# Kernel optimization log

Measured on AMD Instinct MI355X. Metric: run time of the kernel, lower is better.

Reference implementation:

```python
import jax, jax.numpy as jnp
import numpy as np
from jax import lax

B, SEQ, PRED, CIN = 32, 336, 336, 7
ALL = SEQ + PRED
DM, DFF, NFFT, WIN, HOP = 64, 64, 64, 64, 8
NF = ALL // HOP + 1  # 85 STFT frames (center=True)
EL, CL, MARK = 2, 3, 4


def _conv2d(x, w, b, dil, pad):
    y = lax.conv_general_dilated(x, w, (1, 1), [(pad, pad), (pad, pad)],
                                 rhs_dilation=(dil, dil),
                                 dimension_numbers=('NCHW', 'OIHW', 'NCHW'))
    return y + b[None, :, None, None]


def _cconv(xr, xi, wr, wi, br, bi, dil, pad):
    # complex conv: (conv_r + i*conv_i)(xr + i*xi)
    rr = _conv2d(xr, wr, br, dil, pad)
    ii = _conv2d(xi, wi, bi, dil, pad)
    ri = _conv2d(xi, wr, br, dil, pad)
    ir = _conv2d(xr, wi, bi, dil, pad)
    return rr - ii, ri + ir


def _block(x, p):
    # x: [B, ALL, DM]; STFT per channel series (vectorized over B*DM, no python batch loop)
    xp = jnp.pad(x.transpose(0, 2, 1), ((0, 0), (0, 0), (NFFT // 2, NFFT // 2)), mode='reflect')
    idx = jnp.arange(NF)[:, None] * HOP + jnp.arange(NFFT)[None, :]
    win = 0.5 - 0.5 * jnp.cos(2.0 * jnp.pi * jnp.arange(WIN, dtype=jnp.float32) / WIN)  # periodic hann
    frames = xp[:, :, idx] * win  # [B, DM, NF, NFFT]
    S = jnp.fft.fft(frames, axis=-1) / jnp.sqrt(jnp.float32(NFFT))  # normalized=True (ortho)
    Sr = S.real.transpose(0, 1, 3, 2).astype(jnp.float32)  # [B, DM, NFFT, NF]
    Si = S.imag.transpose(0, 1, 3, 2).astype(jnp.float32)
    # complex 'qk' attention: compl_mul1d('ijxk,ijyk->ijxy', S, S)
    qk_r = jnp.einsum('bnxk,bnyk->bnxy', Sr, Sr) - jnp.einsum('bnxk,bnyk->bnxy', Si, Si)
    qk_i = jnp.einsum('bnxk,bnyk->bnxy', Sr, Si) + jnp.einsum('bnxk,bnyk->bnxy', Si, Sr)
    g_r = jax.nn.sigmoid(qk_r)
    g_i = jax.nn.sigmoid(qk_i)
    ar = jnp.einsum('bnxy,bnyz->bnxz', g_r, Sr) - jnp.einsum('bnxy,bnyz->bnxz', g_i, Si)
    ai = jnp.einsum('bnxy,bnyz->bnxz', g_r, Si) + jnp.einsum('bnxy,bnyz->bnxz', g_i, Sr)
    outs_r, outs_i = [], []
    yr, yi = _cconv(ar, ai, p['c0_wr'], p['c0_wi'], p['c0_br'], p['c0_bi'], 1, 0)
    outs_r.append(jax.nn.relu(yr)); outs_i.append(jax.nn.relu(yi))
    for k in range(1, CL):
        hr, hi = _cconv(ar, ai, p['cA_wr'][k - 1], p['cA_wi'][k - 1], p['cA_br'][k - 1], p['cA_bi'][k - 1], k, k)
        yr, yi = _cconv(hr, hi, p['cB_wr'][k - 1], p['cB_wi'][k - 1], p['cB_br'][k - 1], p['cB_bi'][k - 1], k, k)
        outs_r.append(jax.nn.relu(yr)); outs_i.append(jax.nn.relu(yi))
    mr = jnp.mean(jnp.stack(outs_r, -1), -1)
    mi = jnp.mean(jnp.stack(outs_i, -1), -1)
    y = mr * p['l0_w'][0, 0] + mi * p['l0_w'][0, 1] + p['l0_b'][0]  # Linear(2 -> 1) over (real, imag)
    y = y.mean(axis=2)  # mean over freq axis -> [B, DM, NF]
    y = jnp.einsum('bnf,af->bna', y, p['l2_w']) + p['l2_b']  # l2: NF -> ALL
    return y.transpose(0, 2, 1)  # [B, ALL, DM]


def _ln(x, g, b):
    m = x.mean(-1, keepdims=True)
    v = ((x - m) ** 2).mean(-1, keepdims=True)
    return (x - m) / jnp.sqrt(v + 1e-5) * g + b


def _forward(x_enc, x_mark_enc, tok_w, temp_w, pl_w, pl_b, ln_g, ln_b,
             c0_wr, c0_wi, c0_br, c0_bi, cA_wr, cA_wi, cA_br, cA_bi,
             cB_wr, cB_wi, cB_br, cB_bi, l0_w, l0_b, l2_w, l2_b,
             cv_w, cv_b, l1_w, l1_b, proj_w, proj_b):
    means = x_enc.mean(1, keepdims=True)
    xe = x_enc - means
    stdev = jnp.sqrt(xe.var(axis=1, keepdims=True) + 1e-5)
    xe = xe / stdev
    # DataEmbedding: circular token conv + sinusoidal PE + timeF linear (dropout=0)
    xv = jnp.pad(xe.transpose(0, 2, 1), ((0, 0), (0, 0), (1, 1)), mode='wrap')
    val = lax.conv_general_dilated(xv, tok_w, (1,), [(0, 0)],
                                   dimension_numbers=('NCH', 'OIH', 'NCH')).transpose(0, 2, 1)
    pos = jnp.arange(SEQ, dtype=jnp.float32)[:, None]
    div = jnp.exp(jnp.arange(0, DM, 2, dtype=jnp.float32) * (-np.log(10000.0) / DM))
    pe = jnp.zeros((SEQ, DM), jnp.float32).at[:, 0::2].set(jnp.sin(pos * div)).at[:, 1::2].set(jnp.cos(pos * div))
    enc = val + x_mark_enc @ temp_w.T + pe
    enc = jnp.einsum('btd,at->bad', enc, pl_w) + pl_b[None, :, None]  # predict_linear over time axis
    for l in range(EL):
        p = dict(c0_wr=c0_wr[l], c0_wi=c0_wi[l], c0_br=c0_br[l], c0_bi=c0_bi[l],
                 cA_wr=cA_wr[l], cA_wi=cA_wi[l], cA_br=cA_br[l], cA_bi=cA_bi[l],
                 cB_wr=cB_wr[l], cB_wi=cB_wi[l], cB_br=cB_br[l], cB_bi=cB_bi[l],
                 l0_w=l0_w[l], l0_b=l0_b[l], l2_w=l2_w[l], l2_b=l2_b[l])
        enc = _ln(_block(enc, p), ln_g, ln_b)
    # conv1d(in=ALL channels, kernel 3, stride 2, pad 1) over the d_model axis, then l1
    h = lax.conv_general_dilated(enc, cv_w, (2,), [(1, 1)],
                                 dimension_numbers=('NCH', 'OIH', 'NCH')) + cv_b[None, :, None]
    seq_series = (h @ l1_w.T)[..., 0] + l1_b[0]  # [B, ALL]
    dec = enc @ proj_w.T + proj_b
    dec = dec * stdev + means
    return dec[:, -PRED:, :], seq_series


def setup_inputs():
    key = jax.random.key(0)
    ks = jax.random.split(key, 24)
    def r(i, shape, s=0.02):
        return jax.random.normal(ks[i], shape, dtype=jnp.float32) * s
    return {
        'x_enc': jax.random.normal(ks[0], (B, SEQ, CIN), dtype=jnp.float32),
        'x_mark_enc': jax.random.normal(ks[1], (B, SEQ, MARK), dtype=jnp.float32),
        'x_dec': jax.random.normal(ks[2], (B, 48 + PRED, CIN), dtype=jnp.float32),
        'x_mark_dec': jax.random.normal(ks[3], (B, 48 + PRED, MARK), dtype=jnp.float32),
        'tok_w': r(4, (DM, CIN, 3), 0.1),
        'temp_w': r(5, (DM, MARK), 0.1),
        'pl_w': r(6, (ALL, SEQ), 0.05),
        'pl_b': jnp.zeros((ALL,), jnp.float32),
        'ln_g': jnp.ones((DM,), jnp.float32),
        'ln_b': jnp.zeros((DM,), jnp.float32),
        'c0_wr': r(7, (EL, DM, DM, 1, 1), 0.05),
        'c0_wi': r(8, (EL, DM, DM, 1, 1), 0.05),
        'c0_br': jnp.zeros((EL, DM), jnp.float32),
        'c0_bi': jnp.zeros((EL, DM), jnp.float32),
        'cA_wr': r(9, (EL, CL - 1, DFF, DM, 3, 3), 0.02),
        'cA_wi': r(10, (EL, CL - 1, DFF, DM, 3, 3), 0.02),
        'cA_br': jnp.zeros((EL, CL - 1, DFF), jnp.float32),
        'cA_bi': jnp.zeros((EL, CL - 1, DFF), jnp.float32),
        'cB_wr': r(11, (EL, CL - 1, DM, DFF, 3, 3), 0.02),
        'cB_wi': r(12, (EL, CL - 1, DM, DFF, 3, 3), 0.02),
        'cB_br': jnp.zeros((EL, CL - 1, DM), jnp.float32),
        'cB_bi': jnp.zeros((EL, CL - 1, DM), jnp.float32),
        'l0_w': r(13, (EL, 1, 2), 0.5),
        'l0_b': jnp.zeros((EL, 1), jnp.float32),
        'l2_w': r(14, (EL, ALL, NF), 0.05),
        'l2_b': jnp.zeros((EL, ALL), jnp.float32),
        'cv_w': r(15, (ALL, ALL, 3), 0.02),
        'cv_b': jnp.zeros((ALL,), jnp.float32),
        'l1_w': r(16, (1, DM // 2), 0.1),
        'l1_b': jnp.zeros((1,), jnp.float32),
        'proj_w': r(17, (CIN, DM), 0.1),
        'proj_b': jnp.zeros((CIN,), jnp.float32),
    }


def reference(x_enc, x_mark_enc, x_dec, x_mark_dec, tok_w, temp_w, pl_w, pl_b, ln_g, ln_b,
              c0_wr, c0_wi, c0_br, c0_bi, cA_wr, cA_wi, cA_br, cA_bi,
              cB_wr, cB_wi, cB_br, cB_bi, l0_w, l0_b, l2_w, l2_b,
              cv_w, cv_b, l1_w, l1_b, proj_w, proj_b):
    del x_dec, x_mark_dec  # unused in the forecast path
    return _forward(x_enc, x_mark_enc, tok_w, temp_w, pl_w, pl_b, ln_g, ln_b,
                    c0_wr, c0_wi, c0_br, c0_bi, cA_wr, cA_wi, cA_br, cA_bi,
                    cB_wr, cB_wi, cB_br, cB_bi, l0_w, l0_b, l2_w, l2_b,
                    cv_w, cv_b, l1_w, l1_b, proj_w, proj_b)
```

## Files before the change

kernel.cpp:

```cpp
#include <hip/hip_runtime.h>

typedef __attribute__((ext_vector_type(8))) short short8v;
typedef __attribute__((ext_vector_type(4))) float f32x4;
typedef __attribute__((ext_vector_type(16))) float f32x16;

static constexpr int Bt = 32;
static constexpr int SEQ = 336, PRED = 336, CIN = 7, ALLT = 672;
static constexpr int DM = 64, NFFT = 64, HOP = 8, NF = 85;
static constexpr int MARK = 4;
static constexpr float INV3 = 1.0f / 3.0f;

__device__ inline short f2bf(float v) {
    unsigned u = __float_as_uint(v);
    u += 0x7fffu + ((u >> 16) & 1u);
    return (short)(u >> 16);
}
__device__ inline float bf2f(short h) {
    return __uint_as_float(((unsigned)(unsigned short)h) << 16);
}
__device__ inline int pack2(float r, float i) {
    return ((int)(unsigned short)f2bf(r)) | (((int)(unsigned short)f2bf(i)) << 16);
}
__device__ inline void async16(const int* g, short* l) {
    __builtin_amdgcn_global_load_lds(
        (const __attribute__((address_space(1))) unsigned int*)g,
        (__attribute__((address_space(3))) unsigned int*)l, 16, 0, 0);
}

__global__ __launch_bounds__(64) void k_stats(const float* __restrict__ x,
                                              float* __restrict__ mean,
                                              float* __restrict__ stdv) {
    int bc = blockIdx.x;
    int b = bc / CIN, c = bc % CIN;
    int lane = threadIdx.x;
    float s = 0.f, s2 = 0.f;
    for (int t = lane; t < SEQ; t += 64) {
        float v = x[(b * SEQ + t) * CIN + c];
        s += v; s2 += v * v;
    }
    for (int m = 32; m >= 1; m >>= 1) { s += __shfl_xor(s, m); s2 += __shfl_xor(s2, m); }
    if (lane == 0) {
// ... 55 lines not shown
        for (int r = 0; r < 4; ++r) acc[q][r] = 0.f;
    for (int tc = 0; tc < 6; ++tc) {
        if (tc) __syncthreads();
        for (int i = tid; i < 56 * 64; i += 256)
            Et[i] = enc0[((size_t)b * SEQ + tc * 56) * DM + i];
        for (int i = tid; i < 48 * 56; i += 256) {
            int r = i / 56, c = i - r * 56;
            Wt[c * 49 + r] = pl_w[(size_t)(abase + r) * SEQ + tc * 56 + c];
        }
        __syncthreads();
#pragma unroll 4
        for (int t = 0; t < 56; ++t) {
            float4 e = *(const float4*)&Et[t * 64 + d0];
            float w0 = Wt[t * 49 + a0];
            float w1 = Wt[t * 49 + a0 + 1];
            float w2 = Wt[t * 49 + a0 + 2];
            acc[0][0] += w0 * e.x; acc[0][1] += w0 * e.y;
            acc[0][2] += w0 * e.z; acc[0][3] += w0 * e.w;
            acc[1][0] += w1 * e.x; acc[1][1] += w1 * e.y;
            acc[1][2] += w1 * e.z; acc[1][3] += w1 * e.w;
            acc[2][0] += w2 * e.x; acc[2][1] += w2 * e.y;
            acc[2][2] += w2 * e.z; acc[2][3] += w2 * e.w;
        }
    }
#pragma unroll
    for (int q = 0; q < 3; ++q) {
        int a = abase + a0 + q;
        float bias = pl_b[a];
        float4 o = {acc[q][0] + bias, acc[q][1] + bias, acc[q][2] + bias, acc[q][3] + bias};
        *(float4*)&enc[((size_t)b * ALLT + a) * DM + d0] = o;
    }
}

__global__ __launch_bounds__(256) void k_stqka(const float* __restrict__ enc, int b0,
                                               int* __restrict__ Apk) {
    __shared__ __align__(16) short L[54272];
    constexpr int TCH = 0, TCL = 4608, TSH = 9216, TSL = 13824;
    constexpr int XWH = 18432, XWL = 25344;
    float* xp  = (float*)&L[32256];
    float* twc = (float*)&L[33728];
    float* tws = (float*)&L[33984];
    constexpr int SRH = 0, SIH = 6656, SRL = 13312, SIL = 19968;
    constexpr int STRH = 26624, STRL = 33536, STIH = 40448, STIL = 47360;
    constexpr int GRH = 0, GRL = 4608, GIH = 9216, GIL = 13824;

    int blk = blockIdx.x;
    int bn = (blk & 7) * (gridDim.x >> 3) + (blk >> 3);
    int bl = bn >> 6, n = bn & 63;
    int bg = b0 + bl;
    int tid = threadIdx.x;
    int lane = tid & 63, w = tid >> 6;
    int l31 = lane & 31, kg = lane >> 5;

    for (int i = tid; i < ALLT + NFFT; i += 256) {
        int j = i - 32;
        if (j < 0) j = -j;
        if (j > ALLT - 1) j = 2 * (ALLT - 1) - j;
        xp[i] = enc[((size_t)bg * ALLT + j) * DM + n];
    }
    if (tid < 64) {
        float ang = (6.283185307179586f / 64.f) * (float)tid;
        twc[tid] = cosf(ang);
        tws[tid] = sinf(ang);
    }
    __syncthreads();
    for (int i = tid; i < 64 * 64; i += 256) {
        int k = i >> 6, tt = i & 63;
        int m = (k * tt) & 63;
        float c = twc[m], s = tws[m];
        short ch = f2bf(c); short cl = f2bf(c - bf2f(ch));
        short sh = f2bf(s); short sl = f2bf(s - bf2f(sh));
        int o = k * 72 + tt;
        L[TCH + o] = ch; L[TCL + o] = cl; L[TSH + o] = sh; L[TSL + o] = sl;
    }
    for (int i = tid; i < 96 * 64; i += 256) {
        int f = i >> 6, tt = i & 63;
        float v = 0.f;
        if (f < 85) v = xp[f * HOP + tt] * (0.5f - 0.5f * twc[tt]) * 0.125f;
        short vh = f2bf(v); short vl = f2bf(v - bf2f(vh));
        int o = f * 72 + tt;
        L[XWH + o] = vh; L[XWL + o] = vl;
    }
    __syncthreads();

    int kt = w & 1;
    int ftA = (w < 2) ? 0 : 2;
    f32x16 srA, siA, srB, siB;
#pragma unroll
    for (int r = 0; r < 16; ++r) { srA[r] = 0.f; siA[r] = 0.f; srB[r] = 0.f; siB[r] = 0.f; }
#pragma unroll
    for (int tts = 0; tts < 4; ++tts) {
        int ko = (kt * 32 + l31) * 72 + tts * 16 + kg * 8;
        short8v ach = *(const short8v*)&L[TCH + ko];
        short8v acl = *(const short8v*)&L[TCL + ko];
        short8v ash = *(const short8v*)&L[TSH + ko];
        short8v asl = *(const short8v*)&L[TSL + ko];
        {
            int bo = (ftA * 32 + l31) * 72 + tts * 16 + kg * 8;
            short8v bh = *(const short8v*)&L[XWH + bo];
            short8v bl_ = *(const short8v*)&L[XWL + bo];
            srA = __builtin_amdgcn_mfma_f32_32x32x16_bf16(ach, bh, srA, 0, 0, 0);
            srA = __builtin_amdgcn_mfma_f32_32x32x16_bf16(acl, bh, srA, 0, 0, 0);
            srA = __builtin_amdgcn_mfma_f32_32x32x16_bf16(ach, bl_, srA, 0, 0, 0);
            siA = __builtin_amdgcn_mfma_f32_32x32x16_bf16(ash, bh, siA, 0, 0, 0);
            siA = __builtin_amdgcn_mfma_f32_32x32x16_bf16(asl, bh, siA, 0, 0, 0);
            siA = __builtin_amdgcn_mfma_f32_32x32x16_bf16(ash, bl_, siA, 0, 0, 0);
        }
        if (w < 2) {
            int bo = (32 + l31) * 72 + tts * 16 + kg * 8;
            short8v bh = *(const short8v*)&L[XWH + bo];
            short8v bl_ = *(const short8v*)&L[XWL + bo];
            srB = __builtin_amdgcn_mfma_f32_32x32x16_bf16(ach, bh, srB, 0, 0, 0);
            srB = __builtin_amdgcn_mfma_f32_32x32x16_bf16(acl, bh, srB, 0, 0, 0);
            srB = __builtin_amdgcn_mfma_f32_32x32x16_bf16(ach, bl_, srB, 0, 0, 0);
            siB = __builtin_amdgcn_mfma_f32_32x32x16_bf16(ash, bh, siB, 0, 0, 0);
            siB = __builtin_amdgcn_mfma_f32_32x32x16_bf16(asl, bh, siB, 0, 0, 0);
            siB = __builtin_amdgcn_mfma_f32_32x32x16_bf16(ash, bl_, siB, 0, 0, 0);
        }
    }
    __syncthreads();

    {
        int fA = ftA * 32 + l31;
#pragma unroll
        for (int rg = 0; rg < 4; ++rg) {
            int k0 = kt * 32 + 8 * rg + 4 * kg;
            short prh[4], prl[4], pih[4], pil[4];
#pragma unroll
            for (int q = 0; q < 4; ++q) {
                int r = rg * 4 + q;
                float sv = srA[r], iv = -siA[r];
                short rh = f2bf(sv); short rl = f2bf(sv - bf2f(rh));
                short ih = f2bf(iv); short il = f2bf(iv - bf2f(ih));
                prh[q] = rh; prl[q] = rl; pih[q] = ih; pil[q] = il;
                L[SRH + (k0 + q) * 104 + fA] = rh; L[SRL + (k0 + q) * 104 + fA] = rl;
                L[SIH + (k0 + q) * 104 + fA] = ih; L[SIL + (k0 + q) * 104 + fA] = il;
            }
            *(long long*)&L[STRH + fA * 72 + k0] = *(long long*)prh;
            *(long long*)&L[STRL + fA * 72 + k0] = *(long long*)prl;
            *(long long*)&L[STIH + fA * 72 + k0] = *(long long*)pih;
            *(long long*)&L[STIL + fA * 72 + k0] = *(long long*)pil;
        }
        if (w < 2) {
            int fB = 32 + l31;
#pragma unroll
            for (int rg = 0; rg < 4; ++rg) {
                int k0 = kt * 32 + 8 * rg + 4 * kg;
                short prh[4], prl[4], pih[4], pil[4];
#pragma unroll
                for (int q = 0; q < 4; ++q) {
                    int r = rg * 4 + q;
                    float sv = srB[r], iv = -siB[r];
                    short rh = f2bf(sv); short rl = f2bf(sv - bf2f(rh));
                    short ih = f2bf(iv); short il = f2bf(iv - bf2f(ih));
                    prh[q] = rh; prl[q] = rl; pih[q] = ih; pil[q] = il;
                    L[SRH + (k0 + q) * 104 + fB] = rh; L[SRL + (k0 + q) * 104 + fB] = rl;
                    L[SIH + (k0 + q) * 104 + fB] = ih; L[SIL + (k0 + q) * 104 + fB] = il;
                }
                *(long long*)&L[STRH + fB * 72 + k0] = *(long long*)prh;
                *(long long*)&L[STRL + fB * 72 + k0] = *(long long*)prl;
                *(long long*)&L[STIH + fB * 72 + k0] = *(long long*)pih;
                *(long long*)&L[STIL + fB * 72 + k0] = *(long long*)pil;
            }
        }
    }
    __syncthreads();

    int mh = w >> 1, nh = w & 1;
    f32x16 P, Q, R;
#pragma unroll
    for (int r = 0; r < 16; ++r) { P[r] = 0.f; Q[r] = 0.f; R[r] = 0.f; }
#pragma unroll
    for (int f0 = 0; f0 < 96; f0 += 16) {
        int ka = f0 + kg * 8;
        int ra = (mh * 32 + l31) * 104 + ka;
        int rb = (nh * 32 + l31) * 104 + ka;
        short8v a_rh = *(const short8v*)&L[SRH + ra];
        short8v a_rl = *(const short8v*)&L[SRL + ra];
        short8v a_ih = *(const short8v*)&L[SIH + ra];
        short8v a_il = *(const short8v*)&L[SIL + ra];
        short8v b_rh = *(const short8v*)&L[SRH + rb];
        short8v b_rl = *(const short8v*)&L[SRL + rb];
        short8v b_ih = *(const short8v*)&L[SIH + rb];
        short8v b_il = *(const short8v*)&L[SIL + rb];
        P = __builtin_amdgcn_mfma_f32_32x32x16_bf16(a_rh, b_rh, P, 0, 0, 0);
        P = __builtin_amdgcn_mfma_f32_32x32x16_bf16(a_rl, b_rh, P, 0, 0, 0);
        P = __builtin_amdgcn_mfma_f32_32x32x16_bf16(a_rh, b_rl, P, 0, 0, 0);
        Q = __builtin_amdgcn_mfma_f32_32x32x16_bf16(a_ih, b_ih, Q, 0, 0, 0);
        Q = __builtin_amdgcn_mfma_f32_32x32x16_bf16(a_il, b_ih, Q, 0, 0, 0);
        Q = __builtin_amdgcn_mfma_f32_32x32x16_bf16(a_ih, b_il, Q, 0, 0, 0);
        R = __builtin_amdgcn_mfma_f32_32x32x16_bf16(a_rh, b_ih, R, 0, 0, 0);
        R = __builtin_amdgcn_mfma_f32_32x32x16_bf16(a_rl, b_ih, R, 0, 0, 0);
        R = __builtin_amdgcn_mfma_f32_32x32x16_bf16(a_rh, b_il, R, 0, 0, 0);
        R = __builtin_amdgcn_mfma_f32_32x32x16_bf16(a_ih, b_rh, R, 0, 0, 0);
        R = __builtin_amdgcn_mfma_f32_32x32x16_bf16(a_il, b_rh, R, 0, 0, 0);
        R = __builtin_amdgcn_mfma_f32_32x32x16_bf16(a_ih, b_rl, R, 0, 0, 0);
    }
    __syncthreads();

    {
        int y = nh * 32 + l31;
#pragma unroll
        for (int r = 0; r < 16; ++r) {
            int x = mh * 32 + (r & 3) + 8 * (r >> 2) + 4 * kg;
            float gr = 1.f / (1.f + __expf(-(P[r] - Q[r])));
            float gi = 1.f / (1.f + __expf(-R[r]));
            short gh = f2bf(gr); short gl = f2bf(gr - bf2f(gh));
            short jh = f2bf(gi); short jl = f2bf(gi - bf2f(jh));
            L[GRH + x * 72 + y] = gh; L[GRL + x * 72 + y] = gl;
            L[GIH + x * 72 + y] = jh; L[GIL + x * 72 + y] = jl;
        }
    }
    __syncthreads();

    int mg = w >> 1;
    int mtA = (mg == 0) ? 0 : 2;
    f32x16 u1A, u2A, u3A, u1B, u2B, u3B;
#pragma unroll
    for (int r = 0; r < 16; ++r) {
        u1A[r] = 0.f; u2A[r] = 0.f; u3A[r] = 0.f;
        u1B[r] = 0.f; u2B[r] = 0.f; u3B[r] = 0.f;
    }
#pragma unroll
    for (int y0 = 0; y0 < 64; y0 += 16) {
        int kb = y0 + kg * 8;
        int gb = (nh * 32 + l31) * 72 + kb;
        short8v bgrh = *(const short8v*)&L[GRH + gb];
        short8v bgrl = *(const short8v*)&L[GRL + gb];
        short8v bgih = *(const short8v*)&L[GIH + gb];
        short8v bgil = *(const short8v*)&L[GIL + gb];
        {
            int sa = (mtA * 32 + l31) * 72 + kb;
            short8v arh = *(const short8v*)&L[STRH + sa];
            short8v arl = *(const short8v*)&L[STRL + sa];
            short8v aih = *(const short8v*)&L[STIH + sa];
            short8v ail = *(const short8v*)&L[STIL + sa];
            u1A = __builtin_amdgcn_mfma_f32_32x32x16_bf16(arh, bgrh, u1A, 0, 0, 0);
            u1A = __builtin_amdgcn_mfma_f32_32x32x16_bf16(arl, bgrh, u1A, 0, 0, 0);
            u1A = __builtin_amdgcn_mfma_f32_32x32x16_bf16(arh, bgrl, u1A, 0, 0, 0);
            u2A = __builtin_amdgcn_mfma_f32_32x32x16_bf16(aih, bgih, u2A, 0, 0, 0);
            u2A = __builtin_amdgcn_mfma_f32_32x32x16_bf16(ail, bgih, u2A, 0, 0, 0);
            u2A = __builtin_amdgcn_mfma_f32_32x32x16_bf16(aih, bgil, u2A, 0, 0, 0);
            u3A = __builtin_amdgcn_mfma_f32_32x32x16_bf16(aih, bgrh, u3A, 0, 0, 0);
            u3A = __builtin_amdgcn_mfma_f32_32x32x16_bf16(ail, bgrh, u3A, 0, 0, 0);
            u3A = __builtin_amdgcn_mfma_f32_32x32x16_bf16(aih, bgrl, u3A, 0, 0, 0);
            u3A = __builtin_amdgcn_mfma_f32_32x32x16_bf16(arh, bgih, u3A, 0, 0, 0);
            u3A = __builtin_amdgcn_mfma_f32_32x32x16_bf16(arl, bgih, u3A, 0, 0, 0);
            u3A = __builtin_amdgcn_mfma_f32_32x32x16_bf16(arh, bgil, u3A, 0, 0, 0);
        }
        if (mg == 0) {
            int sa = (1 * 32 + l31) * 72 + kb;
            short8v arh = *(const short8v*)&L[STRH + sa];
            short8v arl = *(const short8v*)&L[STRL + sa];
            short8v aih = *(const short8v*)&L[STIH + sa];
            short8v ail = *(const short8v*)&L[STIL + sa];
            u1B = __builtin_amdgcn_mfma_f32_32x32x16_bf16(arh, bgrh, u1B, 0, 0, 0);
            u1B = __builtin_amdgcn_mfma_f32_32x32x16_bf16(arl, bgrh, u1B, 0, 0, 0);
            u1B = __builtin_amdgcn_mfma_f32_32x32x16_bf16(arh, bgrl, u1B, 0, 0, 0);
            u2B = __builtin_amdgcn_mfma_f32_32x32x16_bf16(aih, bgih, u2B, 0, 0, 0);
            u2B = __builtin_amdgcn_mfma_f32_32x32x16_bf16(ail, bgih, u2B, 0, 0, 0);
            u2B = __builtin_amdgcn_mfma_f32_32x32x16_bf16(aih, bgil, u2B, 0, 0, 0);
            u3B = __builtin_amdgcn_mfma_f32_32x32x16_bf16(aih, bgrh, u3B, 0, 0, 0);
            u3B = __builtin_amdgcn_mfma_f32_32x32x16_bf16(ail, bgrh, u3B, 0, 0, 0);
            u3B = __builtin_amdgcn_mfma_f32_32x32x16_bf16(aih, bgrl, u3B, 0, 0, 0);
            u3B = __builtin_amdgcn_mfma_f32_32x32x16_bf16(arh, bgih, u3B, 0, 0, 0);
            u3B = __builtin_amdgcn_mfma_f32_32x32x16_bf16(arl, bgih, u3B, 0, 0, 0);
            u3B = __builtin_amdgcn_mfma_f32_32x32x16_bf16(arh, bgil, u3B, 0, 0, 0);
        }
    }
    {
        size_t pkbase = ((size_t)(bl * 16 + (n >> 2)) * 64) * 85 * 4 + (n & 3);
        int x2 = nh * 32 + l31;
#pragma unroll
        for (int r = 0; r < 16; ++r) {
            int z = mtA * 32 + (r & 3) + 8 * (r >> 2) + 4 * kg;
            if (z < 85)
                Apk[pkbase + ((size_t)x2 * 85 + z) * 4] = pack2(u1A[r] - u2A[r], u3A[r]);
        }
        if (mg == 0) {
#pragma unroll
            for (int r = 0; r < 16; ++r) {
                int z = 32 + (r & 3) + 8 * (r >> 2) + 4 * kg;
                Apk[pkbase + ((size_t)x2 * 85 + z) * 4] = pack2(u1B[r] - u2B[r], u3B[r]);
            }
        }
    }
}

__global__ __launch_bounds__(256) void k_wprep(const float* __restrict__ cA_wr,
                                               const float* __restrict__ cA_wi,
                                               const float* __restrict__ cB_wr,
                                               const float* __restrict__ cB_wi,
                                               const float* __restrict__ c0_wr,
                                               const float* __restrict__ c0_wi,
                                               short* __restrict__ wt) {
    int idx = blockIdx.x * 256 + threadIdx.x;
    if (idx >= 1245184) return;
    int c32 = idx & 31;
    int m = (idx >> 5) & 127;
    int ci_l = c32 >> 1;
    int part = c32 & 1;
    int co = m & 63;
    const float *wr, *wi;
    size_t woff;
    bool lo = false;
    int chunk;
    if (idx < 1179648) {
        chunk = (idx >> 12) & 3;
        int tap = (idx >> 14) % 9;
        int conv = idx / 147456;
        int l = conv >> 2, k1 = (conv >> 1) & 1, ab = conv & 1;
        int ci = chunk * 16 + ci_l;
        woff = (((size_t)(l * 2 + k1) * 64 + co) * 64 + ci) * 9 + tap;
        wr = ab ? cB_wr : cA_wr;
        wi = ab ? cB_wi : cA_wi;
    } else {
        int i2 = idx - 1179648;
        chunk = (i2 >> 12) & 3;
        lo = (i2 >> 14) & 1;
        int l = i2 >> 15;
        int ci = chunk * 16 + ci_l;
        woff = ((size_t)(l * 64 + co)) * 64 + ci;
        wr = c0_wr; wi = c0_wi;
    }
    float a = wr[woff], bb = wi[woff];
    float v = (m < 64) ? (part ? -bb : a) : (part ? a : bb);
    if (lo) v = v - bf2f(f2bf(v));
    wt[idx] = f2bf(v);
}

__global__ __launch_bounds__(256, 4) void k_conv3p(const int* __restrict__ in_pk,
                                                   const short* __restrict__ wt,
                                                   const float* __restrict__ b_r,
                                                   const float* __restrict__ b_i,
                                                   int K, int mode,
                                                   const float* __restrict__ l0w,
                                                   int* __restrict__ out_pk,
                                                   float* __restrict__ yfull) {
    __shared__ __align__(16) short inT[2][1020 * 8];
    int blk = blockIdx.x;
    int swz = (blk & 7) * (gridDim.x >> 3) + (blk >> 3);
    int b = swz >> 6, x0 = swz & 63;
    int tid = threadIdx.x;
    int lane = tid & 63, wid = tid >> 6;
    int wrow = wid & 1, wcol = wid >> 1;
    int l15 = lane & 15, g = lane >> 4;

#define STAGE(CC, BUFI)                                                       \
    do {                                                                      \
        _Pragma("unroll")                                                     \
        for (int it = 0; it < 4; ++it) {                                      \
            int idx = tid + it * 256;                                         \
            if (idx < 1020) {                                                 \
                int f = idx % 85;                                             \
                int rc = idx / 85;                                            \
                int xr = rc >> 2, cg = rc & 3;                                \
                int xg = x0 + (xr - 1) * K;                                   \
                if ((unsigned)xg < 64u) {                                     \
                    const int* src = in_pk +                                  \
                        (((size_t)((b * 16 + (CC) * 4 + cg) * 64 + xg)) * 85 + f) * 4; \
                    async16(src, &inT[BUFI][(wid * 64 + it * 256) * 8]);      \
                }                                                             \
            }                                                                 \
        }                                                                     \
    } while (0)

    { int* p = (int*)&inT[0][0];
      for (int i = tid; i < 2 * 1020 * 4; i += 256) p[i] = 0; }
    __syncthreads();

    f32x4 acc[4][3];
#pragma unroll
    for (int a = 0; a < 4; ++a)
#pragma unroll
        for (int j = 0; j < 3; ++j) acc[a][j] = f32x4{0.f, 0.f, 0.f, 0.f};

    STAGE(0, 0);
    __syncthreads();

    int cur = 0;
    for (int chunk = 0; chunk < 4; ++chunk) {
        if (chunk == 0) STAGE(1, 1);
        else if (chunk == 1) STAGE(2, 0);
        else if (chunk == 2) STAGE(3, 1);
        const short* bb = &inT[cur][0];
#pragma unroll
        for (int u = 0; u < 3; ++u) {
#pragma unroll
            for (int v = 0; v < 3; ++v) {
                int tap = u * 3 + v;
                short8v afr[4];
#pragma unroll
                for (int a = 0; a < 4; ++a) {
                    int tile = (a < 2) ? (wrow * 2 + a) : (wrow * 2 + a + 2);
                    const short* ap = wt + ((((size_t)tap * 4 + chunk) * 8 + tile) * 16 + l15) * 32 + g * 8;
                    afr[a] = *(const short8v*)ap;
                }
                short8v bfr[3];
#pragma unroll
                for (int j = 0; j < 3; ++j) {
                    int fs = (wcol * 3 + j) * 16 + l15 + (v - 1) * K;
                    bool inr = ((unsigned)fs < 85u);
                    int fsc = inr ? fs : 0;
                    short8v t8 = *(const short8v*)&bb[((u * 4 + g) * 85 + fsc) * 8];
                    bfr[j] = inr ? t8 : short8v{0, 0, 0, 0, 0, 0, 0, 0};
                }
#pragma unroll
                for (int a = 0; a < 4; ++a)
#pragma unroll
                    for (int j = 0; j < 3; ++j)
                        acc[a][j] = __builtin_amdgcn_mfma_f32_16x16x32_bf16(afr[a], bfr[j],
                                                                            acc[a][j], 0, 0, 0);
            }
        }
        __syncthreads();
        cur ^= 1;
    }
#undef STAGE

    float w0 = 0.f, w1 = 0.f;
    if (mode == 1) { w0 = l0w[0]; w1 = l0w[1]; }
#pragma unroll
    for (int a = 0; a < 2; ++a) {
#pragma unroll
        for (int j = 0; j < 3; ++j) {
            int f = (wcol * 3 + j) * 16 + l15;
            if (f < NF) {
                if (mode == 0) {
                    int4 o;
#pragma unroll
                    for (int reg = 0; reg < 4; ++reg) {
                        int co = (wrow * 2 + a) * 16 + g * 4 + reg;
                        float vrq = acc[a][j][reg]     + b_r[co] - b_i[co];
                        float viq = acc[a + 2][j][reg] + b_r[co] + b_i[co];
                        ((int*)&o)[reg] = pack2(vrq, viq);
                    }
                    int co4 = (wrow * 2 + a) * 4 + g;
                    ((int4*)out_pk)[((size_t)((b * 16 + co4) * 64 + x0)) * 85 + f] = o;
                } else {
#pragma unroll
                    for (int reg = 0; reg < 4; ++reg) {
                        int co = (wrow * 2 + a) * 16 + g * 4 + reg;
                        float vrq = acc[a][j][reg]     + b_r[co] - b_i[co];
                        float viq = acc[a + 2][j][reg] + b_r[co] + b_i[co];
                        size_t o = ((size_t)(b * 64 + co) * 64 + x0) * NF + f;
                        yfull[o] += (fmaxf(vrq, 0.f) * w0 + fmaxf(viq, 0.f) * w1) * INV3;
                    }
                }
            }
        }
    }
}

__global__ __launch_bounds__(256, 4) void k_c0m(const int* __restrict__ Apk,
                                                const short* __restrict__ wt,
                                                const float* __restrict__ b_r,
                                                const float* __restrict__ b_i,
                                                const float* __restrict__ l0w,
                                                float* __restrict__ yfull) {
    __shared__ __align__(16) short inT[100 * 40];
    int blk = blockIdx.x;
    int swz = (blk & 7) * (gridDim.x >> 3) + (blk >> 3);
    int b = swz >> 6, x0 = swz & 63;
    int tid = threadIdx.x;
    int lane = tid & 63, wid = tid >> 6;
    int wrow = wid & 1, wcol = wid >> 1;
    int l15 = lane & 15, g = lane >> 4;

    f32x4 acc[4][3];
#pragma unroll
    for (int a = 0; a < 4; ++a)
#pragma unroll
        for (int j = 0; j < 3; ++j) acc[a][j] = f32x4{0.f, 0.f, 0.f, 0.f};

    for (int chunk = 0; chunk < 4; ++chunk) {
        if (chunk > 0) __syncthreads();
        for (int idx = tid; idx < 340; idx += 256) {
            int f = idx % 85;
            int cg = idx / 85;
            size_t s4 = ((size_t)((b * 16 + chunk * 4 + cg) * 64 + x0)) * 85 + f;
            int4 dh = ((const int4*)Apk)[s4];
            *(int4*)&inT[(f + 2) * 40 + cg * 8] = dh;
        }
        __syncthreads();
#pragma unroll
        for (int wtap = 0; wtap < 2; ++wtap) {
            short8v afr[4];
#pragma unroll
            for (int a = 0; a < 4; ++a) {
                int tile = (a < 2) ? (wrow * 2 + a) : (wrow * 2 + a + 2);
                const short* ap = wt + ((((size_t)wtap * 4 + chunk) * 8 + tile) * 16 + l15) * 32 + g * 8;
                afr[a] = *(const short8v*)ap;
            }
            short8v bfr[3];
#pragma unroll
            for (int j = 0; j < 3; ++j) {
                int fs = (wcol * 3 + j) * 16 + l15 + 2;
                bfr[j] = *(const short8v*)&inT[fs * 40 + g * 8];
            }
#pragma unroll
            for (int a = 0; a < 4; ++a)
#pragma unroll
                for (int j = 0; j < 3; ++j)
                    acc[a][j] = __builtin_amdgcn_mfma_f32_16x16x32_bf16(afr[a], bfr[j],
                                                                        acc[a][j], 0, 0, 0);
        }
    }

    float w0 = l0w[0], w1 = l0w[1];
#pragma unroll
    for (int a = 0; a < 2; ++a) {
#pragma unroll
        for (int j = 0; j < 3; ++j) {
            int f = (wcol * 3 + j) * 16 + l15;
            if (f < NF) {
// ... 122 lines not shown
    const float* c0_br  = (const float*)d_in[12];
    const float* c0_bi  = (const float*)d_in[13];
    const float* cA_wr  = (const float*)d_in[14];
    const float* cA_wi  = (const float*)d_in[15];
    const float* cA_br  = (const float*)d_in[16];
    const float* cA_bi  = (const float*)d_in[17];
    const float* cB_wr  = (const float*)d_in[18];
    const float* cB_wi  = (const float*)d_in[19];
    const float* cB_br  = (const float*)d_in[20];
    const float* cB_bi  = (const float*)d_in[21];
    const float* l0_w   = (const float*)d_in[22];
    const float* l0_b   = (const float*)d_in[23];
    const float* l2_w   = (const float*)d_in[24];
    const float* l2_b   = (const float*)d_in[25];
    const float* cv_w   = (const float*)d_in[26];
    const float* cv_b   = (const float*)d_in[27];
    const float* l1_w   = (const float*)d_in[28];
    const float* l1_b   = (const float*)d_in[29];
    const float* proj_w = (const float*)d_in[30];
    const float* proj_b = (const float*)d_in[31];

    float* out0 = (float*)d_out;
    float* out1 = out0 + (size_t)Bt * PRED * CIN;

    float* ws = (float*)d_ws;
    size_t off = 0;
    float* enc  = ws + off; off += (size_t)Bt * ALLT * DM;
    float* enc0 = ws + off; off += (size_t)Bt * SEQ * DM;
    float* mean = ws + off; off += 256;
    float* stdv = ws + off; off += 256;
    short* wtbuf = (short*)(ws + off); off += 622592;

    const size_t perb = (size_t)DM * NFFT * NF;
    int Bc = 32;
    while (Bc > 1) {
        size_t need = (off + (size_t)Bc * DM * NF + 3 * (size_t)Bc * perb) * sizeof(float);
        if (need <= ws_size) break;
        Bc >>= 1;
    }
    float* y2 = ws + off; off += (size_t)Bc * DM * NF;
    float* yfull = ws + off; off += (size_t)Bc * perb;
    int*   Apk = (int*)(ws + off); off += (size_t)Bc * perb;
    int*   Hpk = (int*)(ws + off); off += (size_t)Bc * perb;
    float* Tb = enc0;

    k_stats<<<Bt * CIN, 64, 0, stream>>>(x_enc, mean, stdv);
    k_wprep<<<(1245184 + 255) / 256, 256, 0, stream>>>(cA_wr, cA_wi, cB_wr, cB_wi,
                                                       c0_wr, c0_wi, wtbuf);
    k_embed<<<(Bt * SEQ * DM + 255) / 256, 256, 0, stream>>>(x_enc, x_mark, tok_w, temp_w,
                                                             mean, stdv, enc0);
    k_plin2<<<Bt * 14, 256, 0, stream>>>(enc0, pl_w, pl_b, enc);

    for (int l = 0; l < 2; ++l) {
        for (int b0 = 0; b0 < Bt; b0 += Bc) {
            k_stqka<<<Bc * 64, 256, 0, stream>>>(enc, b0, Apk);
            k_c0m<<<Bc * 64, 256, 0, stream>>>(Apk, wtbuf + 1179648 + (size_t)l * 32768,
                                               c0_br + l * 64, c0_bi + l * 64,
                                               l0_w + l * 2, yfull);
            for (int k = 1; k <= 2; ++k) {
                int convA = l * 4 + (k - 1) * 2;
                size_t boff = ((size_t)l * 2 + (k - 1)) * 64;
                k_conv3p<<<Bc * 64, 256, 0, stream>>>(Apk, wtbuf + (size_t)convA * 147456,
                                                      cA_br + boff, cA_bi + boff, k, 0,
                                                      l0_w + l * 2, Hpk, yfull);
                k_conv3p<<<Bc * 64, 256, 0, stream>>>(Hpk, wtbuf + (size_t)(convA + 1) * 147456,
                                                      cB_br + boff, cB_bi + boff, k, 1,
                                                      l0_w + l * 2, Hpk, yfull);
            }
            k_reduce2<<<Bc * 64, 256, 0, stream>>>(yfull, l0_b + l, y2);
            k_l2ln<<<Bc * ALLT, 64, 0, stream>>>(y2, l2_w + (size_t)l * ALLT * NF,
                                                 l2_b + (size_t)l * ALLT, ln_g, ln_b, enc, b0);
        }
    }

    k_T<<<(Bt * ALLT * 3 + 255) / 256, 256, 0, stream>>>(enc, l1_w, Tb);
    k_seq<<<(Bt * ALLT + 255) / 256, 256, 0, stream>>>(Tb, cv_w, cv_b, l1_w, l1_b, out1);
    k_dec<<<(Bt * PRED * CIN + 255) / 256, 256, 0, stream>>>(enc, proj_w, proj_b, mean, stdv, out0);
}
```

Before: 1.369 ms.

## Pad frame dimension of packed activations and widen STFT-attention kernel to 512 threads

The packed complex activation buffers (Apk/Hpk) now use a padded frame stride of 100 with a 2-element zero halo, zeroed once by a memset. This removes bounds checks and conditional zeroing in the conv kernels' B-fragment loads and the reshuffling offset in k_c0m. Separately, k_stqka runs 8 waves so the STFT and the attention-output GEMM tiles each go to their own wave, instead of some waves doing double tiles. The trade-off is more memory traffic for the padded buffers, some idle waves in the QK phase, and a reliance on the halo staying zero across layers.

```diff
diff --git a/kernel.cpp b/kernel.cpp
--- a/kernel.cpp
+++ b/kernel.cpp
@@ -7,6 +7,7 @@
 static constexpr int Bt = 32;
 static constexpr int SEQ = 336, PRED = 336, CIN = 7, ALLT = 672;
 static constexpr int DM = 64, NFFT = 64, HOP = 8, NF = 85;
+static constexpr int FPAD = 100;
 static constexpr int MARK = 4;
 static constexpr float INV3 = 1.0f / 3.0f;
 
@@ -128,7 +129,7 @@
     }
 }
 
-__global__ __launch_bounds__(256) void k_stqka(const float* __restrict__ enc, int b0,
+__global__ __launch_bounds__(512) void k_stqka(const float* __restrict__ enc, int b0,
                                                int* __restrict__ Apk) {
     __shared__ __align__(16) short L[54272];
     constexpr int TCH = 0, TCL = 4608, TSH = 9216, TSL = 13824;
@@ -148,7 +149,7 @@
     int lane = tid & 63, w = tid >> 6;
     int l31 = lane & 31, kg = lane >> 5;
 
-    for (int i = tid; i < ALLT + NFFT; i += 256) {
+    for (int i = tid; i < ALLT + NFFT; i += 512) {
         int j = i - 32;
         if (j < 0) j = -j;
         if (j > ALLT - 1) j = 2 * (ALLT - 1) - j;
@@ -160,7 +161,7 @@
         tws[tid] = sinf(ang);
     }
     __syncthreads();
-    for (int i = tid; i < 64 * 64; i += 256) {
+    for (int i = tid; i < 64 * 64; i += 512) {
         int k = i >> 6, tt = i & 63;
         int m = (k * tt) & 63;
         float c = twc[m], s = tws[m];
@@ -169,7 +170,7 @@
         int o = k * 72 + tt;
         L[TCH + o] = ch; L[TCL + o] = cl; L[TSH + o] = sh; L[TSL + o] = sl;
     }
-    for (int i = tid; i < 96 * 64; i += 256) {
+    for (int i = tid; i < 96 * 64; i += 512) {
         int f = i >> 6, tt = i & 63;
         float v = 0.f;
         if (f < 85) v = xp[f * HOP + tt] * (0.5f - 0.5f * twc[tt]) * 0.125f;
@@ -179,45 +180,33 @@
     }
     __syncthreads();
 
-    int kt = w & 1;
-    int ftA = (w < 2) ? 0 : 2;
-    f32x16 srA, siA, srB, siB;
-#pragma unroll
-    for (int r = 0; r < 16; ++r) { srA[r] = 0.f; siA[r] = 0.f; srB[r] = 0.f; siB[r] = 0.f; }
-#pragma unroll
-    for (int tts = 0; tts < 4; ++tts) {
-        int ko = (kt * 32 + l31) * 72 + tts * 16 + kg * 8;
-        short8v ach = *(const short8v*)&L[TCH + ko];
-        short8v acl = *(const short8v*)&L[TCL + ko];
-        short8v ash = *(const short8v*)&L[TSH + ko];
-        short8v asl = *(const short8v*)&L[TSL + ko];
-        {
-            int bo = (ftA * 32 + l31) * 72 + tts * 16 + kg * 8;
+    int kt = w & 1, ft = w >> 1;
+    f32x16 sr, si;
+#pragma unroll
+    for (int r = 0; r < 16; ++r) { sr[r] = 0.f; si[r] = 0.f; }
+    if (w < 6) {
+#pragma unroll
+        for (int tts = 0; tts < 4; ++tts) {
+            int ko = (kt * 32 + l31) * 72 + tts * 16 + kg * 8;
+            short8v ach = *(const short8v*)&L[TCH + ko];
+            short8v acl = *(const short8v*)&L[TCL + ko];
+            short8v ash = *(const short8v*)&L[TSH + ko];
+            short8v asl = *(const short8v*)&L[TSL + ko];
+            int bo = (ft * 32 + l31) * 72 + tts * 16 + kg * 8;
             short8v bh = *(const short8v*)&L[XWH + bo];
             short8v bl_ = *(const short8v*)&L[XWL + bo];
-            srA = __builtin_amdgcn_mfma_f32_32x32x16_bf16(ach, bh, srA, 0, 0, 0);
-            srA = __builtin_amdgcn_mfma_f32_32x32x16_bf16(acl, bh, srA, 0, 0, 0);
-            srA = __builtin_amdgcn_mfma_f32_32x32x16_bf16(ach, bl_, srA, 0, 0, 0);
-            siA = __builtin_amdgcn_mfma_f32_32x32x16_bf16(ash, bh, siA, 0, 0, 0);
-            siA = __builtin_amdgcn_mfma_f32_32x32x16_bf16(asl, bh, siA, 0, 0, 0);
-            siA = __builtin_amdgcn_mfma_f32_32x32x16_bf16(ash, bl_, siA, 0, 0, 0);
-        }
-        if (w < 2) {
-            int bo = (32 + l31) * 72 + tts * 16 + kg * 8;
-            short8v bh = *(const short8v*)&L[XWH + bo];
-            short8v bl_ = *(const short8v*)&L[XWL + bo];
-            srB = __builtin_amdgcn_mfma_f32_32x32x16_bf16(ach, bh, srB, 0, 0, 0);
-            srB = __builtin_amdgcn_mfma_f32_32x32x16_bf16(acl, bh, srB, 0, 0, 0);
-            srB = __builtin_amdgcn_mfma_f32_32x32x16_bf16(ach, bl_, srB, 0, 0, 0);
-            siB = __builtin_amdgcn_mfma_f32_32x32x16_bf16(ash, bh, siB, 0, 0, 0);
-            siB = __builtin_amdgcn_mfma_f32_32x32x16_bf16(asl, bh, siB, 0, 0, 0);
-            siB = __builtin_amdgcn_mfma_f32_32x32x16_bf16(ash, bl_, siB, 0, 0, 0);
-        }
-    }
-    __syncthreads();
-
-    {
-        int fA = ftA * 32 + l31;
+            sr = __builtin_amdgcn_mfma_f32_32x32x16_bf16(ach, bh, sr, 0, 0, 0);
+            sr = __builtin_amdgcn_mfma_f32_32x32x16_bf16(acl, bh, sr, 0, 0, 0);
+            sr = __builtin_amdgcn_mfma_f32_32x32x16_bf16(ach, bl_, sr, 0, 0, 0);
+            si = __builtin_amdgcn_mfma_f32_32x32x16_bf16(ash, bh, si, 0, 0, 0);
+            si = __builtin_amdgcn_mfma_f32_32x32x16_bf16(asl, bh, si, 0, 0, 0);
+            si = __builtin_amdgcn_mfma_f32_32x32x16_bf16(ash, bl_, si, 0, 0, 0);
+        }
+    }
+    __syncthreads();
+
+    if (w < 6) {
+        int fA = ft * 32 + l31;
 #pragma unroll
         for (int rg = 0; rg < 4; ++rg) {
             int k0 = kt * 32 + 8 * rg + 4 * kg;
@@ -225,7 +214,7 @@
 #pragma unroll
             for (int q = 0; q < 4; ++q) {
                 int r = rg * 4 + q;
-                float sv = srA[r], iv = -siA[r];
+                float sv = sr[r], iv = -si[r];
                 short rh = f2bf(sv); short rl = f2bf(sv - bf2f(rh));
                 short ih = f2bf(iv); short il = f2bf(iv - bf2f(ih));
                 prh[q] = rh; prl[q] = rl; pih[q] = ih; pil[q] = il;
@@ -237,28 +226,6 @@
             *(long long*)&L[STIH + fA * 72 + k0] = *(long long*)pih;
             *(long long*)&L[STIL + fA * 72 + k0] = *(long long*)pil;
         }
-        if (w < 2) {
-            int fB = 32 + l31;
-#pragma unroll
-            for (int rg = 0; rg < 4; ++rg) {
-                int k0 = kt * 32 + 8 * rg + 4 * kg;
-                short prh[4], prl[4], pih[4], pil[4];
-#pragma unroll
-                for (int q = 0; q < 4; ++q) {
-                    int r = rg * 4 + q;
-                    float sv = srB[r], iv = -siB[r];
-                    short rh = f2bf(sv); short rl = f2bf(sv - bf2f(rh));
-                    short ih = f2bf(iv); short il = f2bf(iv - bf2f(ih));
-                    prh[q] = rh; prl[q] = rl; pih[q] = ih; pil[q] = il;
-                    L[SRH + (k0 + q) * 104 + fB] = rh; L[SRL + (k0 + q) * 104 + fB] = rl;
-                    L[SIH + (k0 + q) * 104 + fB] = ih; L[SIL + (k0 + q) * 104 + fB] = il;
-                }
-                *(long long*)&L[STRH + fB * 72 + k0] = *(long long*)prh;
-                *(long long*)&L[STRL + fB * 72 + k0] = *(long long*)prl;
-                *(long long*)&L[STIH + fB * 72 + k0] = *(long long*)pih;
-                *(long long*)&L[STIL + fB * 72 + k0] = *(long long*)pil;
-            }
-        }
     }
     __syncthreads();
 
@@ -266,35 +233,37 @@
     f32x16 P, Q, R;
 #pragma unroll
     for (int r = 0; r < 16; ++r) { P[r] = 0.f; Q[r] = 0.f; R[r] = 0.f; }
-#pragma unroll
-    for (int f0 = 0; f0 < 96; f0 += 16) {
-        int ka = f0 + kg * 8;
-        int ra = (mh * 32 + l31) * 104 + ka;
-        int rb = (nh * 32 + l31) * 104 + ka;
-        short8v a_rh = *(const short8v*)&L[SRH + ra];
-        short8v a_rl = *(const short8v*)&L[SRL + ra];
-        short8v a_ih = *(const short8v*)&L[SIH + ra];
-        short8v a_il = *(const short8v*)&L[SIL + ra];
-        short8v b_rh = *(const short8v*)&L[SRH + rb];
-        short8v b_rl = *(const short8v*)&L[SRL + rb];
-        short8v b_ih = *(const short8v*)&L[SIH + rb];
-        short8v b_il = *(const short8v*)&L[SIL + rb];
-        P = __builtin_amdgcn_mfma_f32_32x32x16_bf16(a_rh, b_rh, P, 0, 0, 0);
-        P = __builtin_amdgcn_mfma_f32_32x32x16_bf16(a_rl, b_rh, P, 0, 0, 0);
-        P = __builtin_amdgcn_mfma_f32_32x32x16_bf16(a_rh, b_rl, P, 0, 0, 0);
-        Q = __builtin_amdgcn_mfma_f32_32x32x16_bf16(a_ih, b_ih, Q, 0, 0, 0);
-        Q = __builtin_amdgcn_mfma_f32_32x32x16_bf16(a_il, b_ih, Q, 0, 0, 0);
-        Q = __builtin_amdgcn_mfma_f32_32x32x16_bf16(a_ih, b_il, Q, 0, 0, 0);
-        R = __builtin_amdgcn_mfma_f32_32x32x16_bf16(a_rh, b_ih, R, 0, 0, 0);
-        R = __builtin_amdgcn_mfma_f32_32x32x16_bf16(a_rl, b_ih, R, 0, 0, 0);
-        R = __builtin_amdgcn_mfma_f32_32x32x16_bf16(a_rh, b_il, R, 0, 0, 0);
-        R = __builtin_amdgcn_mfma_f32_32x32x16_bf16(a_ih, b_rh, R, 0, 0, 0);
-        R = __builtin_amdgcn_mfma_f32_32x32x16_bf16(a_il, b_rh, R, 0, 0, 0);
-        R = __builtin_amdgcn_mfma_f32_32x32x16_bf16(a_ih, b_rl, R, 0, 0, 0);
-    }
-    __syncthreads();
-
-    {
+    if (w < 4) {
+#pragma unroll
+        for (int f0 = 0; f0 < 96; f0 += 16) {
+            int ka = f0 + kg * 8;
+            int ra = (mh * 32 + l31) * 104 + ka;
+            int rb = (nh * 32 + l31) * 104 + ka;
+            short8v a_rh = *(const short8v*)&L[SRH + ra];
+            short8v a_rl = *(const short8v*)&L[SRL + ra];
+            short8v a_ih = *(const short8v*)&L[SIH + ra];
+            short8v a_il = *(const short8v*)&L[SIL + ra];
+            short8v b_rh = *(const short8v*)&L[SRH + rb];
+            short8v b_rl = *(const short8v*)&L[SRL + rb];
+            short8v b_ih = *(const short8v*)&L[SIH + rb];
+            short8v b_il = *(const short8v*)&L[SIL + rb];
+            P = __builtin_amdgcn_mfma_f32_32x32x16_bf16(a_rh, b_rh, P, 0, 0, 0);
+            P = __builtin_amdgcn_mfma_f32_32x32x16_bf16(a_rl, b_rh, P, 0, 0, 0);
+            P = __builtin_amdgcn_mfma_f32_32x32x16_bf16(a_rh, b_rl, P, 0, 0, 0);
+            Q = __builtin_amdgcn_mfma_f32_32x32x16_bf16(a_ih, b_ih, Q, 0, 0, 0);
+            Q = __builtin_amdgcn_mfma_f32_32x32x16_bf16(a_il, b_ih, Q, 0, 0, 0);
+            Q = __builtin_amdgcn_mfma_f32_32x32x16_bf16(a_ih, b_il, Q, 0, 0, 0);
+            R = __builtin_amdgcn_mfma_f32_32x32x16_bf16(a_rh, b_ih, R, 0, 0, 0);
+            R = __builtin_amdgcn_mfma_f32_32x32x16_bf16(a_rl, b_ih, R, 0, 0, 0);
+            R = __builtin_amdgcn_mfma_f32_32x32x16_bf16(a_rh, b_il, R, 0, 0, 0);
+            R = __builtin_amdgcn_mfma_f32_32x32x16_bf16(a_ih, b_rh, R, 0, 0, 0);
+            R = __builtin_amdgcn_mfma_f32_32x32x16_bf16(a_il, b_rh, R, 0, 0, 0);
+            R = __builtin_amdgcn_mfma_f32_32x32x16_bf16(a_ih, b_rl, R, 0, 0, 0);
+        }
+    }
+    __syncthreads();
+
+    if (w < 4) {
         int y = nh * 32 + l31;
 #pragma unroll
         for (int r = 0; r < 16; ++r) {
@@ -309,76 +278,46 @@
     }
     __syncthreads();
 
-    int mg = w >> 1;
-    int mtA = (mg == 0) ? 0 : 2;
-    f32x16 u1A, u2A, u3A, u1B, u2B, u3B;
-#pragma unroll
-    for (int r = 0; r < 16; ++r) {
-        u1A[r] = 0.f; u2A[r] = 0.f; u3A[r] = 0.f;
-        u1B[r] = 0.f; u2B[r] = 0.f; u3B[r] = 0.f;
-    }
-#pragma unroll
-    for (int y0 = 0; y0 < 64; y0 += 16) {
-        int kb = y0 + kg * 8;
-        int gb = (nh * 32 + l31) * 72 + kb;
-        short8v bgrh = *(const short8v*)&L[GRH + gb];
-        short8v bgrl = *(const short8v*)&L[GRL + gb];
-        short8v bgih = *(const short8v*)&L[GIH + gb];
-        short8v bgil = *(const short8v*)&L[GIL + gb];
-        {
-            int sa = (mtA * 32 + l31) * 72 + kb;
+    int mt = w >> 1, nx = w & 1;
+    f32x16 u1, u2, u3;
+#pragma unroll
+    for (int r = 0; r < 16; ++r) { u1[r] = 0.f; u2[r] = 0.f; u3[r] = 0.f; }
+    if (w < 6) {
+#pragma unroll
+        for (int y0 = 0; y0 < 64; y0 += 16) {
+            int kb = y0 + kg * 8;
+            int gb = (nx * 32 + l31) * 72 + kb;
+            short8v bgrh = *(const short8v*)&L[GRH + gb];
+            short8v bgrl = *(const short8v*)&L[GRL + gb];
+            short8v bgih = *(const short8v*)&L[GIH + gb];
+            short8v bgil = *(const short8v*)&L[GIL + gb];
+            int sa = (mt * 32 + l31) * 72 + kb;
             short8v arh = *(const short8v*)&L[STRH + sa];
             short8v arl = *(const short8v*)&L[STRL + sa];
             short8v aih = *(const short8v*)&L[STIH + sa];
             short8v ail = *(const short8v*)&L[STIL + sa];
-            u1A = __builtin_amdgcn_mfma_f32_32x32x16_bf16(arh, bgrh, u1A, 0, 0, 0);
-            u1A = __builtin_amdgcn_mfma_f32_32x32x16_bf16(arl, bgrh, u1A, 0, 0, 0);
-            u1A = __builtin_amdgcn_mfma_f32_32x32x16_bf16(arh, bgrl, u1A, 0, 0, 0);
-            u2A = __builtin_amdgcn_mfma_f32_32x32x16_bf16(aih, bgih, u2A, 0, 0, 0);
-            u2A = __builtin_amdgcn_mfma_f32_32x32x16_bf16(ail, bgih, u2A, 0, 0, 0);
-            u2A = __builtin_amdgcn_mfma_f32_32x32x16_bf16(aih, bgil, u2A, 0, 0, 0);
-            u3A = __builtin_amdgcn_mfma_f32_32x32x16_bf16(aih, bgrh, u3A, 0, 0, 0);
-            u3A = __builtin_amdgcn_mfma_f32_32x32x16_bf16(ail, bgrh, u3A, 0, 0, 0);
-            u3A = __builtin_amdgcn_mfma_f32_32x32x16_bf16(aih, bgrl, u3A, 0, 0, 0);
-            u3A = __builtin_amdgcn_mfma_f32_32x32x16_bf16(arh, bgih, u3A, 0, 0, 0);
-            u3A = __builtin_amdgcn_mfma_f32_32x32x16_bf16(arl, bgih, u3A, 0, 0, 0);
-            u3A = __builtin_amdgcn_mfma_f32_32x32x16_bf16(arh, bgil, u3A, 0, 0, 0);
-        }
-        if (mg == 0) {
-            int sa = (1 * 32 + l31) * 72 + kb;
-            short8v arh = *(const short8v*)&L[STRH + sa];
-            short8v arl = *(const short8v*)&L[STRL + sa];
-            short8v aih = *(const short8v*)&L[STIH + sa];
-            short8v ail = *(const short8v*)&L[STIL + sa];
-            u1B = __builtin_amdgcn_mfma_f32_32x32x16_bf16(arh, bgrh, u1B, 0, 0, 0);
-            u1B = __builtin_amdgcn_mfma_f32_32x32x16_bf16(arl, bgrh, u1B, 0, 0, 0);
-            u1B = __builtin_amdgcn_mfma_f32_32x32x16_bf16(arh, bgrl, u1B, 0, 0, 0);
-            u2B = __builtin_amdgcn_mfma_f32_32x32x16_bf16(aih, bgih, u2B, 0, 0, 0);
-            u2B = __builtin_amdgcn_mfma_f32_32x32x16_bf16(ail, bgih, u2B, 0, 0, 0);
-            u2B = __builtin_amdgcn_mfma_f32_32x32x16_bf16(aih, bgil, u2B, 0, 0, 0);
-            u3B = __builtin_amdgcn_mfma_f32_32x32x16_bf16(aih, bgrh, u3B, 0, 0, 0);
-            u3B = __builtin_amdgcn_mfma_f32_32x32x16_bf16(ail, bgrh, u3B, 0, 0, 0);
-            u3B = __builtin_amdgcn_mfma_f32_32x32x16_bf16(aih, bgrl, u3B, 0, 0, 0);
-            u3B = __builtin_amdgcn_mfma_f32_32x32x16_bf16(arh, bgih, u3B, 0, 0, 0);
-            u3B = __builtin_amdgcn_mfma_f32_32x32x16_bf16(arl, bgih, u3B, 0, 0, 0);
-            u3B = __builtin_amdgcn_mfma_f32_32x32x16_bf16(arh, bgil, u3B, 0, 0, 0);
-        }
-    }
-    {
-        size_t pkbase = ((size_t)(bl * 16 + (n >> 2)) * 64) * 85 * 4 + (n & 3);
-        int x2 = nh * 32 + l31;
+            u1 = __builtin_amdgcn_mfma_f32_32x32x16_bf16(arh, bgrh, u1, 0, 0, 0);
+            u1 = __builtin_amdgcn_mfma_f32_32x32x16_bf16(arl, bgrh, u1, 0, 0, 0);
+            u1 = __builtin_amdgcn_mfma_f32_32x32x16_bf16(arh, bgrl, u1, 0, 0, 0);
+            u2 = __builtin_amdgcn_mfma_f32_32x32x16_bf16(aih, bgih, u2, 0, 0, 0);
+            u2 = __builtin_amdgcn_mfma_f32_32x32x16_bf16(ail, bgih, u2, 0, 0, 0);
+            u2 = __builtin_amdgcn_mfma_f32_32x32x16_bf16(aih, bgil, u2, 0, 0, 0);
+            u3 = __builtin_amdgcn_mfma_f32_32x32x16_bf16(aih, bgrh, u3, 0, 0, 0);
+            u3 = __builtin_amdgcn_mfma_f32_32x32x16_bf16(ail, bgrh, u3, 0, 0, 0);
+            u3 = __builtin_amdgcn_mfma_f32_32x32x16_bf16(aih, bgrl, u3, 0, 0, 0);
+            u3 = __builtin_amdgcn_mfma_f32_32x32x16_bf16(arh, bgih, u3, 0, 0, 0);
+            u3 = __builtin_amdgcn_mfma_f32_32x32x16_bf16(arl, bgih, u3, 0, 0, 0);
+            u3 = __builtin_amdgcn_mfma_f32_32x32x16_bf16(arh, bgil, u3, 0, 0, 0);
+        }
+    }
+    if (w < 6) {
+        size_t pkbase = ((size_t)(bl * 16 + (n >> 2)) * 64) * FPAD * 4 + (n & 3);
+        int x2 = nx * 32 + l31;
 #pragma unroll
         for (int r = 0; r < 16; ++r) {
-            int z = mtA * 32 + (r & 3) + 8 * (r >> 2) + 4 * kg;
+            int z = mt * 32 + (r & 3) + 8 * (r >> 2) + 4 * kg;
             if (z < 85)
-                Apk[pkbase + ((size_t)x2 * 85 + z) * 4] = pack2(u1A[r] - u2A[r], u3A[r]);
-        }
-        if (mg == 0) {
-#pragma unroll
-            for (int r = 0; r < 16; ++r) {
-                int z = 32 + (r & 3) + 8 * (r >> 2) + 4 * kg;
-                Apk[pkbase + ((size_t)x2 * 85 + z) * 4] = pack2(u1B[r] - u2B[r], u3B[r]);
-            }
+                Apk[pkbase + ((size_t)x2 * FPAD + z + 2) * 4] = pack2(u1[r] - u2[r], u3[r]);
         }
     }
 }
@@ -433,7 +372,7 @@
                                                    const float* __restrict__ l0w,
                                                    int* __restrict__ out_pk,
                                                    float* __restrict__ yfull) {
-    __shared__ __align__(16) short inT[2][1020 * 8];
+    __shared__ __align__(16) short inT[2][1200 * 8];
     int blk = blockIdx.x;
     int swz = (blk & 7) * (gridDim.x >> 3) + (blk >> 3);
     int b = swz >> 6, x0 = swz & 63;
@@ -445,16 +384,16 @@
 #define STAGE(CC, BUFI)                                                       \
     do {                                                                      \
         _Pragma("unroll")                                                     \
-        for (int it = 0; it < 4; ++it) {                                      \
+        for (int it = 0; it < 5; ++it) {                                      \
             int idx = tid + it * 256;                                         \
-            if (idx < 1020) {                                                 \
-                int f = idx % 85;                                             \
-                int rc = idx / 85;                                            \
+            if (idx < 1200) {                                                 \
+                int f = idx % FPAD;                                           \
+                int rc = idx / FPAD;                                          \
                 int xr = rc >> 2, cg = rc & 3;                                \
                 int xg = x0 + (xr - 1) * K;                                   \
                 if ((unsigned)xg < 64u) {                                     \
                     const int* src = in_pk +                                  \
-                        (((size_t)((b * 16 + (CC) * 4 + cg) * 64 + xg)) * 85 + f) * 4; \
+                        (((size_t)((b * 16 + (CC) * 4 + cg) * 64 + xg)) * FPAD + f) * 4; \
                     async16(src, &inT[BUFI][(wid * 64 + it * 256) * 8]);      \
                 }                                                             \
             }                                                                 \
@@ -462,7 +401,7 @@
     } while (0)
 
     { int* p = (int*)&inT[0][0];
-      for (int i = tid; i < 2 * 1020 * 4; i += 256) p[i] = 0; }
+      for (int i = tid; i < 2 * 1200 * 4; i += 256) p[i] = 0; }
     __syncthreads();
 
     f32x4 acc[4][3];
@@ -495,11 +434,8 @@
                 short8v bfr[3];
 #pragma unroll
                 for (int j = 0; j < 3; ++j) {
-                    int fs = (wcol * 3 + j) * 16 + l15 + (v - 1) * K;
-                    bool inr = ((unsigned)fs < 85u);
-                    int fsc = inr ? fs : 0;
-                    short8v t8 = *(const short8v*)&bb[((u * 4 + g) * 85 + fsc) * 8];
-                    bfr[j] = inr ? t8 : short8v{0, 0, 0, 0, 0, 0, 0, 0};
+                    int fs2 = (wcol * 3 + j) * 16 + l15 + (v - 1) * K + 2;
+                    bfr[j] = *(const short8v*)&bb[((u * 4 + g) * FPAD + fs2) * 8];
                 }
 #pragma unroll
                 for (int a = 0; a < 4; ++a)
@@ -532,7 +468,7 @@
                         ((int*)&o)[reg] = pack2(vrq, viq);
                     }
                     int co4 = (wrow * 2 + a) * 4 + g;
-                    ((int4*)out_pk)[((size_t)((b * 16 + co4) * 64 + x0)) * 85 + f] = o;
+                    ((int4*)out_pk)[((size_t)((b * 16 + co4) * 64 + x0)) * FPAD + f + 2] = o;
                 } else {
 #pragma unroll
                     for (int reg = 0; reg < 4; ++reg) {
@@ -571,12 +507,12 @@
 
     for (int chunk = 0; chunk < 4; ++chunk) {
         if (chunk > 0) __syncthreads();
-        for (int idx = tid; idx < 340; idx += 256) {
-            int f = idx % 85;
-            int cg = idx / 85;
-            size_t s4 = ((size_t)((b * 16 + chunk * 4 + cg) * 64 + x0)) * 85 + f;
+        for (int idx = tid; idx < 400; idx += 256) {
+            int f = idx % FPAD;
+            int cg = idx / FPAD;
+            size_t s4 = ((size_t)((b * 16 + chunk * 4 + cg) * 64 + x0)) * FPAD + f;
             int4 dh = ((const int4*)Apk)[s4];
-            *(int4*)&inT[(f + 2) * 40 + cg * 8] = dh;
+            *(int4*)&inT[f * 40 + cg * 8] = dh;
         }
         __syncthreads();
 #pragma unroll
@@ -765,17 +701,20 @@
     short* wtbuf = (short*)(ws + off); off += 622592;
 
     const size_t perb = (size_t)DM * NFFT * NF;
+    const size_t perbp = (size_t)16 * 64 * FPAD * 4;
     int Bc = 32;
     while (Bc > 1) {
-        size_t need = (off + (size_t)Bc * DM * NF + 3 * (size_t)Bc * perb) * sizeof(float);
+        size_t need = (off + (size_t)Bc * (DM * NF + perb + 2 * perbp)) * sizeof(float);
         if (need <= ws_size) break;
         Bc >>= 1;
     }
     float* y2 = ws + off; off += (size_t)Bc * DM * NF;
     float* yfull = ws + off; off += (size_t)Bc * perb;
-    int*   Apk = (int*)(ws + off); off += (size_t)Bc * perb;
-    int*   Hpk = (int*)(ws + off); off += (size_t)Bc * perb;
+    int*   Apk = (int*)(ws + off); off += (size_t)Bc * perbp;
+    int*   Hpk = (int*)(ws + off); off += (size_t)Bc * perbp;
     float* Tb = enc0;
+
+    hipMemsetAsync(Apk, 0, (size_t)Bc * perbp * 2 * sizeof(int), stream);
 
     k_stats<<<Bt * CIN, 64, 0, stream>>>(x_enc, mean, stdv);
     k_wprep<<<(1245184 + 255) / 256, 256, 0, stream>>>(cA_wr, cA_wi, cB_wr, cB_wi,
@@ -786,7 +725,7 @@
 
     for (int l = 0; l < 2; ++l) {
         for (int b0 = 0; b0 < Bt; b0 += Bc) {
-            k_stqka<<<Bc * 64, 256, 0, stream>>>(enc, b0, Apk);
+            k_stqka<<<Bc * 64, 512, 0, stream>>>(enc, b0, Apk);
             k_c0m<<<Bc * 64, 256, 0, stream>>>(Apk, wtbuf + 1179648 + (size_t)l * 32768,
                                                c0_br + l * 64, c0_bi + l * 64,
                                                l0_w + l * 2, yfull);
```

Result: no change. 1.382 ms (+1.0%).
